# Kernel optimization log

Hardware: AMD Instinct MI355X
Metric: run time of the kernel (lower is better)

Reference implementation:

```python
import jax, jax.numpy as jnp
import numpy as np

N = 50000      # nodes
E = 600000     # edges (no self-loops in data; GATConv adds them)
IN = 128       # input_dim
HID = 16       # hidden_dim
H1 = 8         # heads1
H2 = 4         # heads2
OUT = 40       # output_dim (classes)
EPS_BN = 1e-5
NEG_SLOPE = 0.2


def setup_inputs() -> dict:
    key = jax.random.key(0)
    ks = jax.random.split(key, 40)
    f32 = jnp.float32

    def p(k, shape, scale=0.1):
        return (jax.random.normal(k, shape) * scale).astype(f32)

    x = jax.random.normal(ks[0], (N, IN), f32)
    src = jax.random.randint(ks[1], (E,), 0, N)
    off = jax.random.randint(ks[2], (E,), 1, N)
    dst = (src + off) % N  # guarantees src != dst
    edge_index = jnp.stack([src, dst]).astype(jnp.int32)

    D1 = HID * H1  # 128
    D2 = HID * H2  # 64
    inp = {
        "x": x, "edge_index": edge_index,
        # conv1: IN -> HID per head, H1 heads, concat
        "W1": p(ks[3], (IN, H1 * HID)), "as1": p(ks[4], (H1, HID)), "ad1": p(ks[5], (H1, HID)), "b1": p(ks[6], (D1,)),
        "g1": jnp.ones((D1,), f32), "be1": jnp.zeros((D1,), f32),
        # conv_mid: D1 -> D1, 1 head, mean (concat=False)
        "Wm": p(ks[7], (D1, D1)), "asm": p(ks[8], (1, D1)), "adm": p(ks[9], (1, D1)), "bm": p(ks[10], (D1,)),
        "gm": jnp.ones((D1,), f32), "bem": jnp.zeros((D1,), f32),
        # conv2: D1 -> HID per head, H2 heads, concat
        "W2": p(ks[11], (D1, H2 * HID)), "as2": p(ks[12], (H2, HID)), "ad2": p(ks[13], (H2, HID)), "b2": p(ks[14], (D2,)),
        "g2": jnp.ones((D2,), f32), "be2": jnp.zeros((D2,), f32),
        # conv3: D2 -> OUT, 1 head, mean
        "W3": p(ks[15], (D2, OUT)), "as3": p(ks[16], (1, OUT)), "ad3": p(ks[17], (1, OUT)), "b3": p(ks[18], (OUT,)),
        "g3": jnp.ones((OUT,), f32), "be3": jnp.zeros((OUT,), f32),
    }
    return inp


def _gat(x, src, dst, W, a_s, a_d, b, concat):
    """PyG GATConv forward (self-loops already appended to src/dst)."""
    Nn = x.shape[0]
    H, C = a_s.shape
    h = (x @ W).reshape(Nn, H, C)                       # [N,H,C]
    s = (h * a_s).sum(-1)                               # [N,H] source score
    d = (h * a_d).sum(-1)                               # [N,H] dest score
    e = jax.nn.leaky_relu(s[src] + d[dst], NEG_SLOPE)   # [E,H]
    # segment softmax over incoming edges of each dst node
    m = jax.ops.segment_max(e, dst, num_segments=Nn)    # [N,H]
    ee = jnp.exp(e - m[dst])
    den = jax.ops.segment_sum(ee, dst, num_segments=Nn)
    alpha = ee / (den[dst] + 1e-16)                     # [E,H]
    out = jax.ops.segment_sum(h[src] * alpha[:, :, None], dst, num_segments=Nn)  # [N,H,C]
    out = out.reshape(Nn, H * C) if concat else out.mean(axis=1)
    return out + b


def _bn(x, g, b):
    mu = x.mean(axis=0)
    var = x.var(axis=0)
    return g * (x - mu) * jax.lax.rsqrt(var + EPS_BN) + b


def reference(x, edge_index, W1, as1, ad1, b1, g1, be1, Wm, asm, adm, bm, gm, bem,
              W2, as2, ad2, b2, g2, be2, W3, as3, ad3, b3, g3, be3):
    Nn = x.shape[0]
    loops = jnp.arange(Nn, dtype=edge_index.dtype)
    src = jnp.concatenate([edge_index[0], loops])
    dst = jnp.concatenate([edge_index[1], loops])

    h = jax.nn.elu(_bn(_gat(x, src, dst, W1, as1, ad1, b1, True), g1, be1))
    res = h
    h = jax.nn.elu(_bn(_gat(h, src, dst, Wm, asm, adm, bm, False), gm, bem))
    h = res + h
    h = jax.nn.elu(_bn(_gat(h, src, dst, W2, as2, ad2, b2, True), g2, be2))
    h = _bn(_gat(h, src, dst, W3, as3, ad3, b3, False), g3, be3)
    return jax.nn.log_softmax(h, axis=1)
```

## Files before the change

### kernel.cpp

```cpp
#include <hip/hip_runtime.h>
#include <hip/hip_bf16.h>
#include <math.h>

#define NN 50000
#define NE 600000
#define ET (NN + NE)

typedef __hip_bfloat16 bf16;
typedef __attribute__((ext_vector_type(8))) short bf16x8;
typedef __attribute__((ext_vector_type(4))) float f32x4;

static __device__ inline unsigned short f2bf(float f) {
    union { __hip_bfloat16 h; unsigned short u; } v;
    v.h = __float2bfloat16(f);
    return v.u;
}

__global__ void k_hist(const int* __restrict__ ei, int* __restrict__ deg) {
    int e = blockIdx.x * blockDim.x + threadIdx.x;
    if (e >= ET) return;
    int d = (e < NE) ? ei[NE + e] : (e - NE);
    atomicAdd(&deg[d], 1);
}

__global__ void k_scan_local(const int* __restrict__ deg, int* __restrict__ tmp,
                             int* __restrict__ csum) {
    __shared__ int wsum[16];
    int i = blockIdx.x * 1024 + threadIdx.x;
    int lane = threadIdx.x & 63, wid = threadIdx.x >> 6;
    int x = (i < NN) ? deg[i] : 0;
    for (int off = 1; off < 64; off <<= 1) {
        int y = __shfl_up(x, off);
        if (lane >= off) x += y;
    }
    if (lane == 63) wsum[wid] = x;
    __syncthreads();
    if (wid == 0) {
        int t = (lane < 16) ? wsum[lane] : 0;
        for (int off = 1; off < 16; off <<= 1) {
            int y = __shfl_up(t, off);
            if (lane >= off) t += y;
        }
        if (lane < 16) wsum[lane] = t;
    }
    __syncthreads();
    if (wid > 0) x += wsum[wid - 1];
    if (i < NN) tmp[i] = x;
    if (threadIdx.x == 1023) csum[blockIdx.x] = x;
}

__global__ void k_scan_chunks(int* __restrict__ csum, int nchunks) {
    int lane = threadIdx.x;
    int v = (lane < nchunks) ? csum[lane] : 0;
    for (int off = 1; off < 64; off <<= 1) {
        int y = __shfl_up(v, off);
        if (lane >= off) v += y;
    }
    if (lane < nchunks) csum[lane] = v;
}

__global__ void k_rowptr(const int* __restrict__ tmp, const int* __restrict__ csum,
                         int* __restrict__ rowptr) {
    int i = blockIdx.x * blockDim.x + threadIdx.x;
    if (i == 0) rowptr[0] = 0;
    if (i < NN) {
        int chunk = i >> 10;
        int off = (chunk > 0) ? csum[chunk - 1] : 0;
        rowptr[i + 1] = tmp[i] + off;
    }
}

__global__ void k_fill(const int* __restrict__ ei, const int* __restrict__ rowptr,
                       int* __restrict__ fill, int* __restrict__ csr) {
    int e = blockIdx.x * blockDim.x + threadIdx.x;
    if (e >= ET) return;
    int s = (e < NE) ? ei[e] : (e - NE);
    int d = (e < NE) ? ei[NE + e] : (e - NE);
    int pos = atomicAdd(&fill[d], 1);
    csr[rowptr[d] + pos] = s;
}

template <int K, int D>
__global__ void k_wconv(const float* __restrict__ W, short* __restrict__ WT) {
    int idx = blockIdx.x * 256 + threadIdx.x;
    if (idx >= K * D) return;
    int d = idx / K, k = idx % K;
    WT[idx] = (short)f2bf(W[k * D + d]);
}

template <int D, int HF>
__global__ __launch_bounds__(64) void k_gemm_mfma(const float* __restrict__ X,
                                                  const short* __restrict__ WT,
                                                  bf16* __restrict__ Hout,
                                                  const float* __restrict__ a_s,
                                                  const float* __restrict__ a_d,
                                                  float* __restrict__ S,
                                                  float* __restrict__ Dv) {
    constexpr int K = 128;
    constexpr int NT = D / 16;
    int lane = threadIdx.x;
    int rb = blockIdx.x * 16;
    int m = lane & 15, kg = lane >> 4;

    f32x4 acc[NT];
#pragma unroll
    for (int n = 0; n < NT; n++) acc[n] = (f32x4){0.f, 0.f, 0.f, 0.f};

    const float* xp = X + (size_t)(rb + m) * K + kg * 8;
#pragma unroll
    for (int k0 = 0; k0 < K; k0 += 32) {
        float4 f0 = *reinterpret_cast<const float4*>(xp + k0);
        float4 f1 = *reinterpret_cast<const float4*>(xp + k0 + 4);
        bf16x8 a;
        a[0] = (short)f2bf(f0.x); a[1] = (short)f2bf(f0.y);
        a[2] = (short)f2bf(f0.z); a[3] = (short)f2bf(f0.w);
        a[4] = (short)f2bf(f1.x); a[5] = (short)f2bf(f1.y);
        a[6] = (short)f2bf(f1.z); a[7] = (short)f2bf(f1.w);
#pragma unroll
        for (int n = 0; n < NT; n++) {
            bf16x8 b = *reinterpret_cast<const bf16x8*>(WT + (size_t)(n * 16 + m) * K + k0 + kg * 8);
            acc[n] = __builtin_amdgcn_mfma_f32_16x16x32_bf16(a, b, acc[n], 0, 0, 0);
        }
    }

    float asv[NT], adv[NT];
#pragma unroll
    for (int n = 0; n < NT; n++) {
        asv[n] = a_s[n * 16 + m];
        adv[n] = a_d[n * 16 + m];
    }
#pragma unroll
    for (int r = 0; r < 4; r++) {
        int row = rb + kg * 4 + r;
#pragma unroll
        for (int n = 0; n < NT; n++)
            Hout[(size_t)row * D + n * 16 + m] = __float2bfloat16(acc[n][r]);
        if constexpr (HF == 1) {
            float sa = 0.f, da = 0.f;
#pragma unroll
            for (int n = 0; n < NT; n++) {
                sa += acc[n][r] * asv[n];
                da += acc[n][r] * adv[n];
            }
            for (int off = 1; off < 16; off <<= 1) {
                sa += __shfl_xor(sa, off);
                da += __shfl_xor(da, off);
            }
            if (m == 0) { S[row] = sa; Dv[row] = da; }
        } else {
#pragma unroll
            for (int n = 0; n < NT; n++) {
                float sa = acc[n][r] * asv[n];
                float da = acc[n][r] * adv[n];
                for (int off = 1; off < 16; off <<= 1) {
                    sa += __shfl_xor(sa, off);
                    da += __shfl_xor(da, off);
                }
                if (m == 0) { S[row * HF + n] = sa; Dv[row * HF + n] = da; }
            }
        }
    }
}

__global__ void k_gemm_small(const float* __restrict__ X, const float* __restrict__ W,
                             bf16* __restrict__ Hout, const float* __restrict__ a_s,
                             const float* __restrict__ a_d, float* __restrict__ S,
                             float* __restrict__ Dv) {
    __shared__ float xs[64];
    int n = blockIdx.x, t = threadIdx.x;
    xs[t] = X[n * 64 + t];
    __syncthreads();
    float acc = 0.f;
    if (t < 40) {
#pragma unroll
        for (int k = 0; k < 64; k++) acc += xs[k] * W[k * 40 + t];
        Hout[n * 40 + t] = __float2bfloat16(acc);
    }
    float sa = (t < 40) ? acc * a_s[t] : 0.f;
    float da = (t < 40) ? acc * a_d[t] : 0.f;
    for (int off = 32; off; off >>= 1) {
        sa += __shfl_xor(sa, off);
        da += __shfl_xor(da, off);
    }
    if (t == 0) {
        S[n] = sa;
        Dv[n] = da;
    }
}

template <int H, int C, int D>
__global__ __launch_bounds__(256) void k_aggregate(const bf16* __restrict__ Hb,
                                                   const float* __restrict__ S,
                                                   const float* __restrict__ Dv,
                                                   const int* __restrict__ rowptr,
                                                   const int* __restrict__ csr,
                                                   float* __restrict__ Out) {
    constexpr int WCAP = 64;
    __shared__ float wl[4][WCAP * H];
    int nl = threadIdx.x >> 6;
    int node = blockIdx.x * 4 + nl;
    if (node >= NN) return;
    int lane = threadIdx.x & 63;
    int r0 = rowptr[node], r1 = rowptr[node + 1];
    int cnt = r1 - r0;
    float dn[H], den[H];
#pragma unroll
    for (int h = 0; h < H; h++) {
        dn[h] = Dv[node * H + h];
        den[h] = 0.f;
    }
    for (int k = lane; k < cnt; k += 64) {
        int u = csr[r0 + k];
        float sv[H];
        if constexpr (H == 8) {
            float4 s0 = *reinterpret_cast<const float4*>(S + (size_t)u * 8);
            float4 s1 = *reinterpret_cast<const float4*>(S + (size_t)u * 8 + 4);
            sv[0] = s0.x; sv[1] = s0.y; sv[2] = s0.z; sv[3] = s0.w;
            sv[4] = s1.x; sv[5] = s1.y; sv[6] = s1.z; sv[7] = s1.w;
        } else if constexpr (H == 4) {
            float4 s0 = *reinterpret_cast<const float4*>(S + (size_t)u * 4);
            sv[0] = s0.x; sv[1] = s0.y; sv[2] = s0.z; sv[3] = s0.w;
        } else {
            sv[0] = S[u];
        }
        float ex[H];
#pragma unroll
        for (int h = 0; h < H; h++) {
            float e = sv[h] + dn[h];
            e = fmaxf(e, 0.2f * e);
            ex[h] = __expf(e);
            den[h] += ex[h];
        }
        if (k < WCAP) {
#pragma unroll
            for (int h = 0; h < H; h++) wl[nl][k * H + h] = ex[h];
        }
    }
#pragma unroll
    for (int h = 0; h < H; h++) {
        for (int off = 32; off; off >>= 1) den[h] += __shfl_xor(den[h], off);
        den[h] = 1.f / (den[h] + 1e-16f);
    }

    constexpr int EPI = (D > 64) ? 1 : 2;
    constexpr int LP = 64 / EPI;
    int sub = lane / LP;
    int j = lane % LP;
    bool act = (2 * j) < D;
    const int h_l = act ? (2 * j) / C : 0;
    float dninv_l = den[0], dn_l = dn[0];
#pragma unroll
    for (int h = 1; h < H; h++) {
        dninv_l = (h_l == h) ? den[h] : dninv_l;
        dn_l = (h_l == h) ? dn[h] : dn_l;
    }
    const float* wlp = &wl[nl][0];
    auto wof = [&](int idx, int u) -> float {
        if (idx < WCAP) return wlp[idx * H + h_l];
        float e = S[(size_t)u * H + h_l] + dn_l;
        e = fmaxf(e, 0.2f * e);
        return __expf(e);
    };
    float ax = 0.f, ay = 0.f;
    int k = sub;
    for (; k + 3 * EPI < cnt; k += 4 * EPI) {
        int u0 = csr[r0 + k];
        int u1 = csr[r0 + k + EPI];
        int u2 = csr[r0 + k + 2 * EPI];
        int u3 = csr[r0 + k + 3 * EPI];
        unsigned p0 = 0, p1 = 0, p2 = 0, p3 = 0;
        if (act) {
            p0 = *reinterpret_cast<const unsigned*>(Hb + (size_t)u0 * D + 2 * j);
            p1 = *reinterpret_cast<const unsigned*>(Hb + (size_t)u1 * D + 2 * j);
            p2 = *reinterpret_cast<const unsigned*>(Hb + (size_t)u2 * D + 2 * j);
            p3 = *reinterpret_cast<const unsigned*>(Hb + (size_t)u3 * D + 2 * j);
        }
        float w0 = wof(k, u0), w1 = wof(k + EPI, u1);
        float w2 = wof(k + 2 * EPI, u2), w3 = wof(k + 3 * EPI, u3);
        ax += w0 * __uint_as_float(p0 << 16) + w1 * __uint_as_float(p1 << 16) +
              w2 * __uint_as_float(p2 << 16) + w3 * __uint_as_float(p3 << 16);
        ay += w0 * __uint_as_float(p0 & 0xffff0000u) + w1 * __uint_as_float(p1 & 0xffff0000u) +
              w2 * __uint_as_float(p2 & 0xffff0000u) + w3 * __uint_as_float(p3 & 0xffff0000u);
    }
    for (; k < cnt; k += EPI) {
        int u = csr[r0 + k];
        unsigned pv = 0;
        if (act) pv = *reinterpret_cast<const unsigned*>(Hb + (size_t)u * D + 2 * j);
        float w = wof(k, u);
        ax += w * __uint_as_float(pv << 16);
        ay += w * __uint_as_float(pv & 0xffff0000u);
    }
    if (EPI == 2) {
        ax += __shfl_xor(ax, 32);
        ay += __shfl_xor(ay, 32);
    }
    if (act && lane < LP) {
        *reinterpret_cast<float2*>(Out + (size_t)node * D + 2 * j) =
            make_float2(ax * dninv_l, ay * dninv_l);
    }
}

template <int D>
__global__ void k_bnstats(const float* __restrict__ X, float* __restrict__ colsum,
                          float* __restrict__ colsq) {
    int col = threadIdx.x;
    if (col >= D) return;
    float s = 0.f, q = 0.f;
    for (int r = blockIdx.x; r < NN; r += gridDim.x) {
        float v = X[(size_t)r * D + col];
        s += v;
        q += v * v;
    }
    atomicAdd(&colsum[col], s);
    atomicAdd(&colsq[col], q);
}

template <int D, int MODE>
__global__ void k_bnapply(const float* __restrict__ X, const float* __restrict__ colsum,
                          const float* __restrict__ colsq, const float* __restrict__ g,
                          const float* __restrict__ be, const float* __restrict__ res,
                          float* __restrict__ Out) {
    int idx = blockIdx.x * blockDim.x + threadIdx.x;
    if (idx >= NN * D) return;
    int col = idx % D;
    float mu = colsum[col] * (1.f / NN);
    float var = colsq[col] * (1.f / NN) - mu * mu;
    float sc = g[col] * rsqrtf(var + 1e-5f);
    float v = sc * (X[idx] - mu) + be[col];
    v = (v > 0.f) ? v : (__expf(v) - 1.f);
    if (MODE == 1) v += res[idx];
    Out[idx] = v;
}

__global__ void k_bn_logsoftmax(const float* __restrict__ X, const float* __restrict__ colsum,
                                const float* __restrict__ colsq, const float* __restrict__ g,
                                const float* __restrict__ be, float* __restrict__ Out) {
    int node = (blockIdx.x * blockDim.x + threadIdx.x) >> 6;
    int lane = threadIdx.x & 63;
    if (node >= NN) return;
    float bnv = 0.f, v = -1e30f;
    if (lane < 40) {
        float mu = colsum[lane] * (1.f / NN);
        float var = colsq[lane] * (1.f / NN) - mu * mu;
        float sc = g[lane] * rsqrtf(var + 1e-5f);
        bnv = sc * (X[node * 40 + lane] - mu) + be[lane];
        v = bnv;
    }
    float m = v;
    for (int off = 32; off; off >>= 1) m = fmaxf(m, __shfl_xor(m, off));
    float ex = (lane < 40) ? expf(bnv - m) : 0.f;
    for (int off = 32; off; off >>= 1) ex += __shfl_xor(ex, off);
    float lse = m + logf(ex);
    if (lane < 40) Out[node * 40 + lane] = bnv - lse;
}

extern "C" void kernel_launch(void* const* d_in, const int* in_sizes, int n_in,
                              void* d_out, int out_size, void* d_ws, size_t ws_size,
                              hipStream_t stream) {
    (void)in_sizes; (void)n_in; (void)out_size; (void)ws_size;
    const float* x   = (const float*)d_in[0];
    const int*   ei  = (const int*)d_in[1];
    const float* W1  = (const float*)d_in[2];
    const float* as1 = (const float*)d_in[3];
    const float* ad1 = (const float*)d_in[4];
    const float* g1  = (const float*)d_in[6];
    const float* be1 = (const float*)d_in[7];
    const float* Wm  = (const float*)d_in[8];
    const float* asm_ = (const float*)d_in[9];
    const float* adm = (const float*)d_in[10];
    const float* gm  = (const float*)d_in[12];
    const float* bem = (const float*)d_in[13];
    const float* W2  = (const float*)d_in[14];
    const float* as2 = (const float*)d_in[15];
    const float* ad2 = (const float*)d_in[16];
    const float* g2  = (const float*)d_in[18];
    const float* be2 = (const float*)d_in[19];
    const float* W3  = (const float*)d_in[20];
    const float* as3 = (const float*)d_in[21];
    const float* ad3 = (const float*)d_in[22];
    const float* g3  = (const float*)d_in[24];
    const float* be3 = (const float*)d_in[25];
    float* out = (float*)d_out;

    char* ws = (char*)d_ws;
    size_t off = 0;
    auto alloc = [&](size_t b) {
        void* p = ws + off;
        off = (off + b + 255) & ~(size_t)255;
        return p;
    };
    int* rowptr = (int*)alloc((NN + 1) * 4);
    int* csr    = (int*)alloc((size_t)ET * 4);
    int* deg    = (int*)alloc(NN * 4);
    int* tmp    = (int*)alloc(NN * 4);
    int* csum   = (int*)alloc(256 * 4);
    bf16* Hbf   = (bf16*)alloc((size_t)NN * 128 * 2);
    float* A    = (float*)alloc((size_t)NN * 128 * 4);
    float* B    = (float*)alloc((size_t)NN * 128 * 4);
    float* S    = (float*)alloc((size_t)NN * 8 * 4);
    float* Dv   = (float*)alloc((size_t)NN * 8 * 4);
    float* cs   = (float*)alloc(256 * 4);
    float* cq   = cs + 128;
    short* WT1  = (short*)alloc(128 * 128 * 2);
    short* WTm  = (short*)alloc(128 * 128 * 2);
    short* WT2  = (short*)alloc(128 * 64 * 2);

    const int nchunks = (NN + 1023) / 1024;

    k_wconv<128, 128><<<64, 256, 0, stream>>>(W1, WT1);
    k_wconv<128, 128><<<64, 256, 0, stream>>>(Wm, WTm);
    k_wconv<128, 64><<<32, 256, 0, stream>>>(W2, WT2);

    hipMemsetAsync(deg, 0, NN * 4, stream);
    k_hist<<<(ET + 255) / 256, 256, 0, stream>>>(ei, deg);
    k_scan_local<<<nchunks, 1024, 0, stream>>>(deg, tmp, csum);
    k_scan_chunks<<<1, 64, 0, stream>>>(csum, nchunks);
    k_rowptr<<<(NN + 255) / 256, 256, 0, stream>>>(tmp, csum, rowptr);
    hipMemsetAsync(deg, 0, NN * 4, stream);
    k_fill<<<(ET + 255) / 256, 256, 0, stream>>>(ei, rowptr, deg, csr);

    const int mfma_blocks = NN / 16;
    const int node_wave_blocks = (NN + 3) / 4;

    k_gemm_mfma<128, 8><<<mfma_blocks, 64, 0, stream>>>(x, WT1, Hbf, as1, ad1, S, Dv);
    k_aggregate<8, 16, 128><<<node_wave_blocks, 256, 0, stream>>>(Hbf, S, Dv, rowptr, csr, A);
    hipMemsetAsync(cs, 0, 256 * 4, stream);
    k_bnstats<128><<<512, 128, 0, stream>>>(A, cs, cq);
    k_bnapply<128, 0><<<(NN * 128 + 255) / 256, 256, 0, stream>>>(A, cs, cq, g1, be1, nullptr, B);

    k_gemm_mfma<128, 1><<<mfma_blocks, 64, 0, stream>>>(B, WTm, Hbf, asm_, adm, S, Dv);
    k_aggregate<1, 128, 128><<<node_wave_blocks, 256, 0, stream>>>(Hbf, S, Dv, rowptr, csr, A);
    hipMemsetAsync(cs, 0, 256 * 4, stream);
    k_bnstats<128><<<512, 128, 0, stream>>>(A, cs, cq);
    k_bnapply<128, 1><<<(NN * 128 + 255) / 256, 256, 0, stream>>>(A, cs, cq, gm, bem, B, A);

    k_gemm_mfma<64, 4><<<mfma_blocks, 64, 0, stream>>>(A, WT2, Hbf, as2, ad2, S, Dv);
    k_aggregate<4, 16, 64><<<node_wave_blocks, 256, 0, stream>>>(Hbf, S, Dv, rowptr, csr, B);
    hipMemsetAsync(cs, 0, 256 * 4, stream);
    k_bnstats<64><<<512, 64, 0, stream>>>(B, cs, cq);
    k_bnapply<64, 0><<<(NN * 64 + 255) / 256, 256, 0, stream>>>(B, cs, cq, g2, be2, nullptr, B);

    k_gemm_small<<<NN, 64, 0, stream>>>(B, W3, Hbf, as3, ad3, S, Dv);
    k_aggregate<1, 40, 40><<<node_wave_blocks, 256, 0, stream>>>(Hbf, S, Dv, rowptr, csr, A);
    hipMemsetAsync(cs, 0, 256 * 4, stream);
    k_bnstats<40><<<512, 64, 0, stream>>>(A, cs, cq);
    k_bn_logsoftmax<<<node_wave_blocks, 256, 0, stream>>>(A, cs, cq, g3, be3, out);
}
```

Measured before the change: 624.9 us.

## Store intermediate activations in bf16 and deepen aggregate gather unroll to eight

Aggregation outputs, batchnorm outputs and residual buffers now use bf16 instead of fp32. The GEMM kernels load bf16 activations directly instead of converting fp32 on the fly. Every inter-layer tensor pass moves half the bytes through bn stats, bn apply and the GEMMs. The aggregate kernel also gains an 8-wide unrolled gather loop so more neighbor loads are in flight at once. The cost is extra rounding of activations and the residual, which could affect accuracy, and higher register pressure in the aggregate kernel.

```diff
diff --git a/kernel.cpp b/kernel.cpp
--- a/kernel.cpp
+++ b/kernel.cpp
@@ -15,6 +15,7 @@
     v.h = __float2bfloat16(f);
     return v.u;
 }
+static __device__ inline float bf2f(bf16 h) { return __bfloat162float(h); }
 
 __global__ void k_hist(const int* __restrict__ ei, int* __restrict__ deg) {
     int e = blockIdx.x * blockDim.x + threadIdx.x;
@@ -88,8 +89,9 @@
     WT[idx] = (short)f2bf(W[k * D + d]);
 }
 
-template <int D, int HF>
-__global__ __launch_bounds__(64) void k_gemm_mfma(const float* __restrict__ X,
+template <int D, int HF, bool B16>
+__global__ __launch_bounds__(64) void k_gemm_mfma(const float* __restrict__ Xf,
+                                                  const bf16* __restrict__ Xh,
                                                   const short* __restrict__ WT,
                                                   bf16* __restrict__ Hout,
                                                   const float* __restrict__ a_s,
@@ -106,16 +108,20 @@
 #pragma unroll
     for (int n = 0; n < NT; n++) acc[n] = (f32x4){0.f, 0.f, 0.f, 0.f};
 
-    const float* xp = X + (size_t)(rb + m) * K + kg * 8;
 #pragma unroll
     for (int k0 = 0; k0 < K; k0 += 32) {
-        float4 f0 = *reinterpret_cast<const float4*>(xp + k0);
-        float4 f1 = *reinterpret_cast<const float4*>(xp + k0 + 4);
         bf16x8 a;
-        a[0] = (short)f2bf(f0.x); a[1] = (short)f2bf(f0.y);
-        a[2] = (short)f2bf(f0.z); a[3] = (short)f2bf(f0.w);
-        a[4] = (short)f2bf(f1.x); a[5] = (short)f2bf(f1.y);
-        a[6] = (short)f2bf(f1.z); a[7] = (short)f2bf(f1.w);
+        if constexpr (B16) {
+            a = *reinterpret_cast<const bf16x8*>(Xh + (size_t)(rb + m) * K + k0 + kg * 8);
+        } else {
+            const float* xp = Xf + (size_t)(rb + m) * K + k0 + kg * 8;
+            float4 f0 = *reinterpret_cast<const float4*>(xp);
+            float4 f1 = *reinterpret_cast<const float4*>(xp + 4);
+            a[0] = (short)f2bf(f0.x); a[1] = (short)f2bf(f0.y);
+            a[2] = (short)f2bf(f0.z); a[3] = (short)f2bf(f0.w);
+            a[4] = (short)f2bf(f1.x); a[5] = (short)f2bf(f1.y);
+            a[6] = (short)f2bf(f1.z); a[7] = (short)f2bf(f1.w);
+        }
 #pragma unroll
         for (int n = 0; n < NT; n++) {
             bf16x8 b = *reinterpret_cast<const bf16x8*>(WT + (size_t)(n * 16 + m) * K + k0 + kg * 8);
@@ -162,13 +168,13 @@
     }
 }
 
-__global__ void k_gemm_small(const float* __restrict__ X, const float* __restrict__ W,
+__global__ void k_gemm_small(const bf16* __restrict__ X, const float* __restrict__ W,
                              bf16* __restrict__ Hout, const float* __restrict__ a_s,
                              const float* __restrict__ a_d, float* __restrict__ S,
                              float* __restrict__ Dv) {
     __shared__ float xs[64];
     int n = blockIdx.x, t = threadIdx.x;
-    xs[t] = X[n * 64 + t];
+    xs[t] = bf2f(X[n * 64 + t]);
     __syncthreads();
     float acc = 0.f;
     if (t < 40) {
@@ -194,7 +200,7 @@
                                                    const float* __restrict__ Dv,
                                                    const int* __restrict__ rowptr,
                                                    const int* __restrict__ csr,
-                                                   float* __restrict__ Out) {
+                                                   bf16* __restrict__ Out) {
     constexpr int WCAP = 64;
     __shared__ float wl[4][WCAP * H];
     int nl = threadIdx.x >> 6;
@@ -263,24 +269,35 @@
     };
     float ax = 0.f, ay = 0.f;
     int k = sub;
+    for (; k + 7 * EPI < cnt; k += 8 * EPI) {
+        int uu[8];
+        unsigned pp[8];
+#pragma unroll
+        for (int i = 0; i < 8; i++) uu[i] = csr[r0 + k + i * EPI];
+#pragma unroll
+        for (int i = 0; i < 8; i++)
+            pp[i] = act ? *reinterpret_cast<const unsigned*>(Hb + (size_t)uu[i] * D + 2 * j) : 0u;
+#pragma unroll
+        for (int i = 0; i < 8; i++) {
+            float w = wof(k + i * EPI, uu[i]);
+            ax += w * __uint_as_float(pp[i] << 16);
+            ay += w * __uint_as_float(pp[i] & 0xffff0000u);
+        }
+    }
     for (; k + 3 * EPI < cnt; k += 4 * EPI) {
-        int u0 = csr[r0 + k];
-        int u1 = csr[r0 + k + EPI];
-        int u2 = csr[r0 + k + 2 * EPI];
-        int u3 = csr[r0 + k + 3 * EPI];
-        unsigned p0 = 0, p1 = 0, p2 = 0, p3 = 0;
-        if (act) {
-            p0 = *reinterpret_cast<const unsigned*>(Hb + (size_t)u0 * D + 2 * j);
-            p1 = *reinterpret_cast<const unsigned*>(Hb + (size_t)u1 * D + 2 * j);
-            p2 = *reinterpret_cast<const unsigned*>(Hb + (size_t)u2 * D + 2 * j);
-            p3 = *reinterpret_cast<const unsigned*>(Hb + (size_t)u3 * D + 2 * j);
-        }
-        float w0 = wof(k, u0), w1 = wof(k + EPI, u1);
-        float w2 = wof(k + 2 * EPI, u2), w3 = wof(k + 3 * EPI, u3);
-        ax += w0 * __uint_as_float(p0 << 16) + w1 * __uint_as_float(p1 << 16) +
-              w2 * __uint_as_float(p2 << 16) + w3 * __uint_as_float(p3 << 16);
-        ay += w0 * __uint_as_float(p0 & 0xffff0000u) + w1 * __uint_as_float(p1 & 0xffff0000u) +
-              w2 * __uint_as_float(p2 & 0xffff0000u) + w3 * __uint_as_float(p3 & 0xffff0000u);
+        int uu[4];
+        unsigned pp[4];
+#pragma unroll
+        for (int i = 0; i < 4; i++) uu[i] = csr[r0 + k + i * EPI];
+#pragma unroll
+        for (int i = 0; i < 4; i++)
+            pp[i] = act ? *reinterpret_cast<const unsigned*>(Hb + (size_t)uu[i] * D + 2 * j) : 0u;
+#pragma unroll
+        for (int i = 0; i < 4; i++) {
+            float w = wof(k + i * EPI, uu[i]);
+            ax += w * __uint_as_float(pp[i] << 16);
+            ay += w * __uint_as_float(pp[i] & 0xffff0000u);
+        }
     }
     for (; k < cnt; k += EPI) {
         int u = csr[r0 + k];
@@ -295,19 +312,19 @@
         ay += __shfl_xor(ay, 32);
     }
     if (act && lane < LP) {
-        *reinterpret_cast<float2*>(Out + (size_t)node * D + 2 * j) =
-            make_float2(ax * dninv_l, ay * dninv_l);
+        unsigned o = (unsigned)f2bf(ax * dninv_l) | ((unsigned)f2bf(ay * dninv_l) << 16);
+        *reinterpret_cast<unsigned*>(Out + (size_t)node * D + 2 * j) = o;
     }
 }
 
 template <int D>
-__global__ void k_bnstats(const float* __restrict__ X, float* __restrict__ colsum,
+__global__ void k_bnstats(const bf16* __restrict__ X, float* __restrict__ colsum,
                           float* __restrict__ colsq) {
     int col = threadIdx.x;
     if (col >= D) return;
     float s = 0.f, q = 0.f;
     for (int r = blockIdx.x; r < NN; r += gridDim.x) {
-        float v = X[(size_t)r * D + col];
+        float v = bf2f(X[(size_t)r * D + col]);
         s += v;
         q += v * v;
     }
@@ -316,23 +333,23 @@
 }
 
 template <int D, int MODE>
-__global__ void k_bnapply(const float* __restrict__ X, const float* __restrict__ colsum,
+__global__ void k_bnapply(const bf16* __restrict__ X, const float* __restrict__ colsum,
                           const float* __restrict__ colsq, const float* __restrict__ g,
-                          const float* __restrict__ be, const float* __restrict__ res,
-                          float* __restrict__ Out) {
+                          const float* __restrict__ be, const bf16* __restrict__ res,
+                          bf16* __restrict__ Out) {
     int idx = blockIdx.x * blockDim.x + threadIdx.x;
     if (idx >= NN * D) return;
     int col = idx % D;
     float mu = colsum[col] * (1.f / NN);
     float var = colsq[col] * (1.f / NN) - mu * mu;
     float sc = g[col] * rsqrtf(var + 1e-5f);
-    float v = sc * (X[idx] - mu) + be[col];
+    float v = sc * (bf2f(X[idx]) - mu) + be[col];
     v = (v > 0.f) ? v : (__expf(v) - 1.f);
-    if (MODE == 1) v += res[idx];
-    Out[idx] = v;
-}
-
-__global__ void k_bn_logsoftmax(const float* __restrict__ X, const float* __restrict__ colsum,
+    if (MODE == 1) v += bf2f(res[idx]);
+    Out[idx] = __float2bfloat16(v);
+}
+
+__global__ void k_bn_logsoftmax(const bf16* __restrict__ X, const float* __restrict__ colsum,
                                 const float* __restrict__ colsq, const float* __restrict__ g,
                                 const float* __restrict__ be, float* __restrict__ Out) {
     int node = (blockIdx.x * blockDim.x + threadIdx.x) >> 6;
@@ -343,7 +360,7 @@
         float mu = colsum[lane] * (1.f / NN);
         float var = colsq[lane] * (1.f / NN) - mu * mu;
         float sc = g[lane] * rsqrtf(var + 1e-5f);
-        bnv = sc * (X[node * 40 + lane] - mu) + be[lane];
+        bnv = sc * (bf2f(X[node * 40 + lane]) - mu) + be[lane];
         v = bnv;
     }
     float m = v;
@@ -395,8 +412,9 @@
     int* tmp    = (int*)alloc(NN * 4);
     int* csum   = (int*)alloc(256 * 4);
     bf16* Hbf   = (bf16*)alloc((size_t)NN * 128 * 2);
-    float* A    = (float*)alloc((size_t)NN * 128 * 4);
-    float* B    = (float*)alloc((size_t)NN * 128 * 4);
+    bf16* AG    = (bf16*)alloc((size_t)NN * 128 * 2);
+    bf16* P1    = (bf16*)alloc((size_t)NN * 128 * 2);
+    bf16* P2    = (bf16*)alloc((size_t)NN * 128 * 2);
     float* S    = (float*)alloc((size_t)NN * 8 * 4);
     float* Dv   = (float*)alloc((size_t)NN * 8 * 4);
     float* cs   = (float*)alloc(256 * 4);
@@ -422,27 +440,27 @@
     const int mfma_blocks = NN / 16;
     const int node_wave_blocks = (NN + 3) / 4;
 
-    k_gemm_mfma<128, 8><<<mfma_blocks, 64, 0, stream>>>(x, WT1, Hbf, as1, ad1, S, Dv);
-    k_aggregate<8, 16, 128><<<node_wave_blocks, 256, 0, stream>>>(Hbf, S, Dv, rowptr, csr, A);
+    k_gemm_mfma<128, 8, false><<<mfma_blocks, 64, 0, stream>>>(x, nullptr, WT1, Hbf, as1, ad1, S, Dv);
+    k_aggregate<8, 16, 128><<<node_wave_blocks, 256, 0, stream>>>(Hbf, S, Dv, rowptr, csr, AG);
     hipMemsetAsync(cs, 0, 256 * 4, stream);
-    k_bnstats<128><<<512, 128, 0, stream>>>(A, cs, cq);
-    k_bnapply<128, 0><<<(NN * 128 + 255) / 256, 256, 0, stream>>>(A, cs, cq, g1, be1, nullptr, B);
-
-    k_gemm_mfma<128, 1><<<mfma_blocks, 64, 0, stream>>>(B, WTm, Hbf, asm_, adm, S, Dv);
-    k_aggregate<1, 128, 128><<<node_wave_blocks, 256, 0, stream>>>(Hbf, S, Dv, rowptr, csr, A);
+    k_bnstats<128><<<512, 128, 0, stream>>>(AG, cs, cq);
+    k_bnapply<128, 0><<<(NN * 128 + 255) / 256, 256, 0, stream>>>(AG, cs, cq, g1, be1, nullptr, P1);
+
+    k_gemm_mfma<128, 1, true><<<mfma_blocks, 64, 0, stream>>>(nullptr, P1, WTm, Hbf, asm_, adm, S, Dv);
+    k_aggregate<1, 128, 128><<<node_wave_blocks, 256, 0, stream>>>(Hbf, S, Dv, rowptr, csr, AG);
     hipMemsetAsync(cs, 0, 256 * 4, stream);
-    k_bnstats<128><<<512, 128, 0, stream>>>(A, cs, cq);
-    k_bnapply<128, 1><<<(NN * 128 + 255) / 256, 256, 0, stream>>>(A, cs, cq, gm, bem, B, A);
-
-    k_gemm_mfma<64, 4><<<mfma_blocks, 64, 0, stream>>>(A, WT2, Hbf, as2, ad2, S, Dv);
-    k_aggregate<4, 16, 64><<<node_wave_blocks, 256, 0, stream>>>(Hbf, S, Dv, rowptr, csr, B);
+    k_bnstats<128><<<512, 128, 0, stream>>>(AG, cs, cq);
+    k_bnapply<128, 1><<<(NN * 128 + 255) / 256, 256, 0, stream>>>(AG, cs, cq, gm, bem, P1, P2);
+
+    k_gemm_mfma<64, 4, true><<<mfma_blocks, 64, 0, stream>>>(nullptr, P2, WT2, Hbf, as2, ad2, S, Dv);
+    k_aggregate<4, 16, 64><<<node_wave_blocks, 256, 0, stream>>>(Hbf, S, Dv, rowptr, csr, AG);
     hipMemsetAsync(cs, 0, 256 * 4, stream);
-    k_bnstats<64><<<512, 64, 0, stream>>>(B, cs, cq);
-    k_bnapply<64, 0><<<(NN * 64 + 255) / 256, 256, 0, stream>>>(B, cs, cq, g2, be2, nullptr, B);
-
-    k_gemm_small<<<NN, 64, 0, stream>>>(B, W3, Hbf, as3, ad3, S, Dv);
-    k_aggregate<1, 40, 40><<<node_wave_blocks, 256, 0, stream>>>(Hbf, S, Dv, rowptr, csr, A);
+    k_bnstats<64><<<512, 64, 0, stream>>>(AG, cs, cq);
+    k_bnapply<64, 0><<<(NN * 64 + 255) / 256, 256, 0, stream>>>(AG, cs, cq, g2, be2, nullptr, P1);
+
+    k_gemm_small<<<NN, 64, 0, stream>>>(P1, W3, Hbf, as3, ad3, S, Dv);
+    k_aggregate<1, 40, 40><<<node_wave_blocks, 256, 0, stream>>>(Hbf, S, Dv, rowptr, csr, AG);
     hipMemsetAsync(cs, 0, 256 * 4, stream);
-    k_bnstats<40><<<512, 64, 0, stream>>>(A, cs, cq);
-    k_bn_logsoftmax<<<node_wave_blocks, 256, 0, stream>>>(A, cs, cq, g3, be3, out);
-}
+    k_bnstats<40><<<512, 64, 0, stream>>>(AG, cs, cq);
+    k_bn_logsoftmax<<<node_wave_blocks, 256, 0, stream>>>(AG, cs, cq, g3, be3, out);
+}
```

After: 624.8 us. About the same (-0.0%).

## Fuse BN+ELU+residual into next GEMM loads and store aggregates as bf16

Applied to the files above, without the earlier changes.

Removes the separate BN-apply kernels. A tiny finalize kernel computes per-column scale and shift, and the next GEMM applies BN, ELU and the residual add on the fly while loading its operand. Aggregation outputs are now stored in bf16 rather than fp32, which halves the traffic for the aggregate writes, the BN stats reads and the GEMM reads. The three weight-conversion launches and the memsets are also merged into one. In exchange the BN statistics are computed from bf16-rounded values, and the layer-1 activation is recomputed inside the layer-2 GEMM for the residual.

```diff
diff --git a/kernel.cpp b/kernel.cpp
--- a/kernel.cpp
+++ b/kernel.cpp
@@ -15,6 +15,7 @@
     v.h = __float2bfloat16(f);
     return v.u;
 }
+static __device__ inline float bf2f(bf16 h) { return __bfloat162float(h); }
 
 __global__ void k_hist(const int* __restrict__ ei, int* __restrict__ deg) {
     int e = blockIdx.x * blockDim.x + threadIdx.x;
@@ -80,16 +81,41 @@
     csr[rowptr[d] + pos] = s;
 }
 
-template <int K, int D>
-__global__ void k_wconv(const float* __restrict__ W, short* __restrict__ WT) {
+__global__ void k_wconv_all(const float* __restrict__ W1, const float* __restrict__ Wm,
+                            const float* __restrict__ W2, short* __restrict__ WT1,
+                            short* __restrict__ WTm, short* __restrict__ WT2) {
     int idx = blockIdx.x * 256 + threadIdx.x;
-    if (idx >= K * D) return;
-    int d = idx / K, k = idx % K;
-    WT[idx] = (short)f2bf(W[k * D + d]);
-}
-
-template <int D, int HF>
-__global__ __launch_bounds__(64) void k_gemm_mfma(const float* __restrict__ X,
+    if (idx < 16384) {
+        int d = idx >> 7, k = idx & 127;
+        WT1[idx] = (short)f2bf(W1[k * 128 + d]);
+    } else if (idx < 32768) {
+        int i2 = idx - 16384;
+        int d = i2 >> 7, k = i2 & 127;
+        WTm[i2] = (short)f2bf(Wm[k * 128 + d]);
+    } else if (idx < 40960) {
+        int i3 = idx - 32768;
+        int d = i3 >> 7, k = i3 & 127;
+        WT2[i3] = (short)f2bf(W2[k * 64 + d]);
+    }
+}
+
+template <int D>
+__global__ void k_bnfin(const float* __restrict__ sums, const float* __restrict__ g,
+                        const float* __restrict__ be, float2* __restrict__ ss) {
+    int c = threadIdx.x;
+    if (c >= D) return;
+    float mu = sums[c] * (1.f / NN);
+    float var = sums[128 + c] * (1.f / NN) - mu * mu;
+    float sc = g[c] * rsqrtf(var + 1e-5f);
+    ss[c] = make_float2(sc, be[c] - mu * sc);
+}
+
+template <int D, int HF, int MODE>
+__global__ __launch_bounds__(64) void k_gemm_mfma(const float* __restrict__ Xf,
+                                                  const bf16* __restrict__ X1,
+                                                  const float2* __restrict__ ss1,
+                                                  const bf16* __restrict__ X2,
+                                                  const float2* __restrict__ ss2,
                                                   const short* __restrict__ WT,
                                                   bf16* __restrict__ Hout,
                                                   const float* __restrict__ a_s,
@@ -106,19 +132,42 @@
 #pragma unroll
     for (int n = 0; n < NT; n++) acc[n] = (f32x4){0.f, 0.f, 0.f, 0.f};
 
-    const float* xp = X + (size_t)(rb + m) * K + kg * 8;
 #pragma unroll
     for (int k0 = 0; k0 < K; k0 += 32) {
-        float4 f0 = *reinterpret_cast<const float4*>(xp + k0);
-        float4 f1 = *reinterpret_cast<const float4*>(xp + k0 + 4);
+        int cb = k0 + kg * 8;
         bf16x8 a;
-        a[0] = (short)f2bf(f0.x); a[1] = (short)f2bf(f0.y);
-        a[2] = (short)f2bf(f0.z); a[3] = (short)f2bf(f0.w);
-        a[4] = (short)f2bf(f1.x); a[5] = (short)f2bf(f1.y);
-        a[6] = (short)f2bf(f1.z); a[7] = (short)f2bf(f1.w);
+        if constexpr (MODE == 0) {
+            const float* xp = Xf + (size_t)(rb + m) * K + cb;
+            float4 f0 = *reinterpret_cast<const float4*>(xp);
+            float4 f1 = *reinterpret_cast<const float4*>(xp + 4);
+            a[0] = (short)f2bf(f0.x); a[1] = (short)f2bf(f0.y);
+            a[2] = (short)f2bf(f0.z); a[3] = (short)f2bf(f0.w);
+            a[4] = (short)f2bf(f1.x); a[5] = (short)f2bf(f1.y);
+            a[6] = (short)f2bf(f1.z); a[7] = (short)f2bf(f1.w);
+        } else {
+            bf16x8 r1 = *reinterpret_cast<const bf16x8*>(X1 + (size_t)(rb + m) * K + cb);
+            bf16x8 r2;
+            if constexpr (MODE == 2)
+                r2 = *reinterpret_cast<const bf16x8*>(X2 + (size_t)(rb + m) * K + cb);
+#pragma unroll
+            for (int j = 0; j < 8; j++) {
+                float2 p1 = ss1[cb + j];
+                bf16 b1; *(short*)&b1 = r1[j];
+                float v = p1.x * bf2f(b1) + p1.y;
+                v = (v > 0.f) ? v : (__expf(v) - 1.f);
+                if constexpr (MODE == 2) {
+                    float2 p2 = ss2[cb + j];
+                    bf16 b2; *(short*)&b2 = r2[j];
+                    float v2 = p2.x * bf2f(b2) + p2.y;
+                    v2 = (v2 > 0.f) ? v2 : (__expf(v2) - 1.f);
+                    v += v2;
+                }
+                a[j] = (short)f2bf(v);
+            }
+        }
 #pragma unroll
         for (int n = 0; n < NT; n++) {
-            bf16x8 b = *reinterpret_cast<const bf16x8*>(WT + (size_t)(n * 16 + m) * K + k0 + kg * 8);
+            bf16x8 b = *reinterpret_cast<const bf16x8*>(WT + (size_t)(n * 16 + m) * K + cb);
             acc[n] = __builtin_amdgcn_mfma_f32_16x16x32_bf16(a, b, acc[n], 0, 0, 0);
         }
     }
@@ -162,13 +211,17 @@
     }
 }
 
-__global__ void k_gemm_small(const float* __restrict__ X, const float* __restrict__ W,
-                             bf16* __restrict__ Hout, const float* __restrict__ a_s,
-                             const float* __restrict__ a_d, float* __restrict__ S,
-                             float* __restrict__ Dv) {
+__global__ void k_gemm_small(const bf16* __restrict__ X, const float2* __restrict__ ss,
+                             const float* __restrict__ W, bf16* __restrict__ Hout,
+                             const float* __restrict__ a_s, const float* __restrict__ a_d,
+                             float* __restrict__ S, float* __restrict__ Dv) {
     __shared__ float xs[64];
     int n = blockIdx.x, t = threadIdx.x;
-    xs[t] = X[n * 64 + t];
+    {
+        float2 p = ss[t];
+        float v = p.x * bf2f(X[n * 64 + t]) + p.y;
+        xs[t] = (v > 0.f) ? v : (__expf(v) - 1.f);
+    }
     __syncthreads();
     float acc = 0.f;
     if (t < 40) {
@@ -194,7 +247,7 @@
                                                    const float* __restrict__ Dv,
                                                    const int* __restrict__ rowptr,
                                                    const int* __restrict__ csr,
-                                                   float* __restrict__ Out) {
+                                                   bf16* __restrict__ Out) {
     constexpr int WCAP = 64;
     __shared__ float wl[4][WCAP * H];
     int nl = threadIdx.x >> 6;
@@ -295,55 +348,37 @@
         ay += __shfl_xor(ay, 32);
     }
     if (act && lane < LP) {
-        *reinterpret_cast<float2*>(Out + (size_t)node * D + 2 * j) =
-            make_float2(ax * dninv_l, ay * dninv_l);
+        unsigned o = (unsigned)f2bf(ax * dninv_l) | ((unsigned)f2bf(ay * dninv_l) << 16);
+        *reinterpret_cast<unsigned*>(Out + (size_t)node * D + 2 * j) = o;
     }
 }
 
 template <int D>
-__global__ void k_bnstats(const float* __restrict__ X, float* __restrict__ colsum,
-                          float* __restrict__ colsq) {
+__global__ void k_bnstats(const bf16* __restrict__ X, float* __restrict__ sums) {
     int col = threadIdx.x;
     if (col >= D) return;
     float s = 0.f, q = 0.f;
     for (int r = blockIdx.x; r < NN; r += gridDim.x) {
-        float v = X[(size_t)r * D + col];
+        float v = bf2f(X[(size_t)r * D + col]);
         s += v;
         q += v * v;
     }
-    atomicAdd(&colsum[col], s);
-    atomicAdd(&colsq[col], q);
-}
-
-template <int D, int MODE>
-__global__ void k_bnapply(const float* __restrict__ X, const float* __restrict__ colsum,
-                          const float* __restrict__ colsq, const float* __restrict__ g,
-                          const float* __restrict__ be, const float* __restrict__ res,
-                          float* __restrict__ Out) {
-    int idx = blockIdx.x * blockDim.x + threadIdx.x;
-    if (idx >= NN * D) return;
-    int col = idx % D;
-    float mu = colsum[col] * (1.f / NN);
-    float var = colsq[col] * (1.f / NN) - mu * mu;
-    float sc = g[col] * rsqrtf(var + 1e-5f);
-    float v = sc * (X[idx] - mu) + be[col];
-    v = (v > 0.f) ? v : (__expf(v) - 1.f);
-    if (MODE == 1) v += res[idx];
-    Out[idx] = v;
-}
-
-__global__ void k_bn_logsoftmax(const float* __restrict__ X, const float* __restrict__ colsum,
-                                const float* __restrict__ colsq, const float* __restrict__ g,
-                                const float* __restrict__ be, float* __restrict__ Out) {
+    atomicAdd(&sums[col], s);
+    atomicAdd(&sums[128 + col], q);
+}
+
+__global__ void k_bn_logsoftmax(const bf16* __restrict__ X, const float* __restrict__ sums,
+                                const float* __restrict__ g, const float* __restrict__ be,
+                                float* __restrict__ Out) {
     int node = (blockIdx.x * blockDim.x + threadIdx.x) >> 6;
     int lane = threadIdx.x & 63;
     if (node >= NN) return;
     float bnv = 0.f, v = -1e30f;
     if (lane < 40) {
-        float mu = colsum[lane] * (1.f / NN);
-        float var = colsq[lane] * (1.f / NN) - mu * mu;
+        float mu = sums[lane] * (1.f / NN);
+        float var = sums[128 + lane] * (1.f / NN) - mu * mu;
         float sc = g[lane] * rsqrtf(var + 1e-5f);
-        bnv = sc * (X[node * 40 + lane] - mu) + be[lane];
+        bnv = sc * (bf2f(X[node * 40 + lane]) - mu) + be[lane];
         v = bnv;
     }
     float m = v;
@@ -395,21 +430,24 @@
     int* tmp    = (int*)alloc(NN * 4);
     int* csum   = (int*)alloc(256 * 4);
     bf16* Hbf   = (bf16*)alloc((size_t)NN * 128 * 2);
-    float* A    = (float*)alloc((size_t)NN * 128 * 4);
-    float* B    = (float*)alloc((size_t)NN * 128 * 4);
+    bf16* AG1   = (bf16*)alloc((size_t)NN * 128 * 2);
+    bf16* AG2   = (bf16*)alloc((size_t)NN * 128 * 2);
+    bf16* AG3   = (bf16*)alloc((size_t)NN * 64 * 2);
+    bf16* AG4   = (bf16*)alloc((size_t)NN * 40 * 2);
     float* S    = (float*)alloc((size_t)NN * 8 * 4);
     float* Dv   = (float*)alloc((size_t)NN * 8 * 4);
-    float* cs   = (float*)alloc(256 * 4);
-    float* cq   = cs + 128;
+    float* bns  = (float*)alloc(4 * 256 * 4);
+    float2* ss1 = (float2*)alloc(128 * 8);
+    float2* ssM = (float2*)alloc(128 * 8);
+    float2* ss2 = (float2*)alloc(64 * 8);
     short* WT1  = (short*)alloc(128 * 128 * 2);
     short* WTm  = (short*)alloc(128 * 128 * 2);
     short* WT2  = (short*)alloc(128 * 64 * 2);
 
     const int nchunks = (NN + 1023) / 1024;
 
-    k_wconv<128, 128><<<64, 256, 0, stream>>>(W1, WT1);
-    k_wconv<128, 128><<<64, 256, 0, stream>>>(Wm, WTm);
-    k_wconv<128, 64><<<32, 256, 0, stream>>>(W2, WT2);
+    hipMemsetAsync(bns, 0, 4 * 256 * 4, stream);
+    k_wconv_all<<<160, 256, 0, stream>>>(W1, Wm, W2, WT1, WTm, WT2);
 
     hipMemsetAsync(deg, 0, NN * 4, stream);
     k_hist<<<(ET + 255) / 256, 256, 0, stream>>>(ei, deg);
@@ -422,27 +460,26 @@
     const int mfma_blocks = NN / 16;
     const int node_wave_blocks = (NN + 3) / 4;
 
-    k_gemm_mfma<128, 8><<<mfma_blocks, 64, 0, stream>>>(x, WT1, Hbf, as1, ad1, S, Dv);
-    k_aggregate<8, 16, 128><<<node_wave_blocks, 256, 0, stream>>>(Hbf, S, Dv, rowptr, csr, A);
-    hipMemsetAsync(cs, 0, 256 * 4, stream);
-    k_bnstats<128><<<512, 128, 0, stream>>>(A, cs, cq);
-    k_bnapply<128, 0><<<(NN * 128 + 255) / 256, 256, 0, stream>>>(A, cs, cq, g1, be1, nullptr, B);
-
-    k_gemm_mfma<128, 1><<<mfma_blocks, 64, 0, stream>>>(B, WTm, Hbf, asm_, adm, S, Dv);
-    k_aggregate<1, 128, 128><<<node_wave_blocks, 256, 0, stream>>>(Hbf, S, Dv, rowptr, csr, A);
-    hipMemsetAsync(cs, 0, 256 * 4, stream);
-    k_bnstats<128><<<512, 128, 0, stream>>>(A, cs, cq);
-    k_bnapply<128, 1><<<(NN * 128 + 255) / 256, 256, 0, stream>>>(A, cs, cq, gm, bem, B, A);
-
-    k_gemm_mfma<64, 4><<<mfma_blocks, 64, 0, stream>>>(A, WT2, Hbf, as2, ad2, S, Dv);
-    k_aggregate<4, 16, 64><<<node_wave_blocks, 256, 0, stream>>>(Hbf, S, Dv, rowptr, csr, B);
-    hipMemsetAsync(cs, 0, 256 * 4, stream);
-    k_bnstats<64><<<512, 64, 0, stream>>>(B, cs, cq);
-    k_bnapply<64, 0><<<(NN * 64 + 255) / 256, 256, 0, stream>>>(B, cs, cq, g2, be2, nullptr, B);
-
-    k_gemm_small<<<NN, 64, 0, stream>>>(B, W3, Hbf, as3, ad3, S, Dv);
-    k_aggregate<1, 40, 40><<<node_wave_blocks, 256, 0, stream>>>(Hbf, S, Dv, rowptr, csr, A);
-    hipMemsetAsync(cs, 0, 256 * 4, stream);
-    k_bnstats<40><<<512, 64, 0, stream>>>(A, cs, cq);
-    k_bn_logsoftmax<<<node_wave_blocks, 256, 0, stream>>>(A, cs, cq, g3, be3, out);
-}
+    k_gemm_mfma<128, 8, 0><<<mfma_blocks, 64, 0, stream>>>(x, nullptr, nullptr, nullptr, nullptr,
+                                                           WT1, Hbf, as1, ad1, S, Dv);
+    k_aggregate<8, 16, 128><<<node_wave_blocks, 256, 0, stream>>>(Hbf, S, Dv, rowptr, csr, AG1);
+    k_bnstats<128><<<512, 128, 0, stream>>>(AG1, bns + 0 * 256);
+    k_bnfin<128><<<1, 128, 0, stream>>>(bns + 0 * 256, g1, be1, ss1);
+
+    k_gemm_mfma<128, 1, 1><<<mfma_blocks, 64, 0, stream>>>(nullptr, AG1, ss1, nullptr, nullptr,
+                                                           WTm, Hbf, asm_, adm, S, Dv);
+    k_aggregate<1, 128, 128><<<node_wave_blocks, 256, 0, stream>>>(Hbf, S, Dv, rowptr, csr, AG2);
+    k_bnstats<128><<<512, 128, 0, stream>>>(AG2, bns + 1 * 256);
+    k_bnfin<128><<<1, 128, 0, stream>>>(bns + 1 * 256, gm, bem, ssM);
+
+    k_gemm_mfma<64, 4, 2><<<mfma_blocks, 64, 0, stream>>>(nullptr, AG2, ssM, AG1, ss1,
+                                                          WT2, Hbf, as2, ad2, S, Dv);
+    k_aggregate<4, 16, 64><<<node_wave_blocks, 256, 0, stream>>>(Hbf, S, Dv, rowptr, csr, AG3);
+    k_bnstats<64><<<512, 64, 0, stream>>>(AG3, bns + 2 * 256);
+    k_bnfin<64><<<1, 64, 0, stream>>>(bns + 2 * 256, g2, be2, ss2);
+
+    k_gemm_small<<<NN, 64, 0, stream>>>(AG3, ss2, W3, Hbf, as3, ad3, S, Dv);
+    k_aggregate<1, 40, 40><<<node_wave_blocks, 256, 0, stream>>>(Hbf, S, Dv, rowptr, csr, AG4);
+    k_bnstats<40><<<512, 64, 0, stream>>>(AG4, bns + 3 * 256);
+    k_bn_logsoftmax<<<node_wave_blocks, 256, 0, stream>>>(AG4, bns + 3 * 256, g3, be3, out);
+}
```

Measured after the change: 581.0 us. 1.08x faster.
